# Kernel tuning notes

Hardware: AMD Instinct MI355X
Metric: run time of the kernel (lower is better)

The kernel has to match this reference:

```python
import jax, jax.numpy as jnp
import numpy as np

MEM_SIZE = 2000
FEA_DIM = 256
FMAP = 32
BATCH = 32
SHRINK = 0.0025
EPS = 1e-12


def setup_inputs() -> dict:
    key = jax.random.key(0)
    k1, k2, k3, k4 = jax.random.split(key, 4)
    stdv = 1.0 / np.sqrt(FEA_DIM)
    inp = {
        "input": jax.random.normal(k1, (BATCH, FEA_DIM, FMAP, FMAP), dtype=jnp.float32),
        "label_batch": jax.random.randint(k2, (BATCH,), 0, 2),
        "weight": jax.random.uniform(k3, (MEM_SIZE, FEA_DIM), dtype=jnp.float32, minval=-stdv, maxval=stdv),
        "pos_embedding": jax.random.normal(k4, (1, FEA_DIM, FMAP, FMAP), dtype=jnp.float32),
    }
    return inp


def _forward(x, weight, pos_embedding):
    b, c, h, w = x.shape
    m = weight.shape[0]
    x = x + pos_embedding  # pos=True
    xr = x.transpose(0, 2, 3, 1).reshape(-1, c)  # [b*h*w, c]
    # addressing: linear -> softmax over memory slots
    att = jax.nn.softmax(jnp.einsum('nc,mc->nm', xr, weight), axis=1)  # [N, m]
    # compact loss: MSE to nearest memory item (argmax of att before shrink)
    idx = jnp.argmax(att, axis=1)
    pos_item = weight[idx]  # [N, c]
    compact_loss = jnp.mean((xr - pos_item) ** 2)
    # distance loss: hinge on pairwise squared distances between memory items
    sq = jnp.sum(weight * weight, axis=1)
    d2 = sq[:, None] + sq[None, :] - 2.0 * (weight @ weight.T)  # [m, m]
    dist = 1.0 - d2
    dist = dist * (dist > 0).astype(dist.dtype)
    dist = jnp.triu(dist, k=1)
    distance_loss = dist.sum() * 2.0 / (m * (m - 1))
    # hard shrink relu + L1 normalize (shrink_thres > 0)
    att = jax.nn.relu(att - SHRINK) * att / (jnp.abs(att - SHRINK) + EPS)
    att = att / jnp.maximum(jnp.sum(jnp.abs(att), axis=1, keepdims=True), EPS)
    # memory read
    out = jnp.einsum('nm,mc->nc', att, weight)
    out = out.reshape(b, h, w, c).transpose(0, 3, 1, 2)
    return out, compact_loss, distance_loss


def reference(input, label_batch, weight, pos_embedding):
    return _forward(input, weight, pos_embedding)
```

## Files before the change

kernel.cpp:

```cpp
#include <hip/hip_runtime.h>
#include <hip/hip_bf16.h>

typedef unsigned char u8;
typedef unsigned short u16;
typedef unsigned int u32;
typedef long long s64;
typedef float f32x4 __attribute__((ext_vector_type(4)));
typedef long long s64x2 __attribute__((ext_vector_type(2)));

#define MEM    2000
#define FEA    256
#define SLSTR  2064
#define OSTR   265
#define XRS    264
#define XRBASE 98304
#define RING2  66048
#define POOLSZ 131584
#define OUTN   8388608

typedef const __attribute__((address_space(1))) u32* gp1;
typedef __attribute__((address_space(3))) u32* lp3;

__device__ __forceinline__ void gl_lds16(const void* g, void* l) {
    __builtin_amdgcn_global_load_lds((gp1)g, (lp3)l, 16, 0, 0);
}
__device__ __forceinline__ void pipe_bar() {
    __builtin_amdgcn_sched_barrier(0);
    __builtin_amdgcn_s_barrier();
    __builtin_amdgcn_sched_barrier(0);
}
__device__ __forceinline__ void lds_bar() {
    asm volatile("s_waitcnt lgkmcnt(0)" ::: "memory");
    pipe_bar();
}

__device__ __forceinline__ u32 f2e4m3(float x) {
    float ax = fabsf(x);
    u32 s = (__builtin_bit_cast(u32, x) >> 24) & 0x80u;
    if (ax >= 448.f) return s | 0x7e;
    if (ax < 0.015625f) {
        int q = (int)rintf(ax * 512.f);
        return s | (u32)q;
    }
    int e = (int)(__builtin_bit_cast(u32, ax) >> 23) - 127;
    float scale = __builtin_bit_cast(float, (u32)((127 - e + 3) << 23));
    int q = (int)rintf(ax * scale);
    int E = e + 7;
    if (q == 16) { q = 8; E += 1; if (E > 15) return s | 0x7e; }
    return s | (u32)(E << 3) | (u32)(q & 7);
}
__device__ __forceinline__ u32 f2e4m3_fast(float v) {
    u32 u = __builtin_bit_cast(u32, v);
    u += 0x0007FFFFu + ((u >> 20) & 1u);
    int bb = (int)(u >> 20) - 0x3C0;
    return bb < 0 ? 0u : (u32)bb;
}

__global__ __launch_bounds__(256) void prep_kernel(const float* __restrict__ W,
                                                   u8* __restrict__ WTc,
                                                   u8* __restrict__ Wc,
                                                   float* __restrict__ sqv,
                                                   float* __restrict__ loss) {
    const int blk = blockIdx.x, t = threadIdx.x;
    const int m0 = blk * 8;
    {
        const int sl = t >> 5, cl = t & 31;
        const int slot = m0 + sl;
        const int ch0 = cl * 8;
        const float* wr = W + slot * 256 + ch0;
        f32x4 v0 = *(const f32x4*)wr;
        f32x4 v1 = *(const f32x4*)(wr + 4);
        float ss = v0[0]*v0[0] + v0[1]*v0[1] + v0[2]*v0[2] + v0[3]*v0[3]
                 + v1[0]*v1[0] + v1[1]*v1[1] + v1[2]*v1[2] + v1[3]*v1[3];
        ss += __shfl_xor(ss, 1); ss += __shfl_xor(ss, 2); ss += __shfl_xor(ss, 4);
        ss += __shfl_xor(ss, 8); ss += __shfl_xor(ss, 16);
        if (cl == 0) sqv[slot] = ss;
        const int c = slot >> 6, s = slot & 63;
        const int kk = cl >> 2, agp = cl & 3;
        const int kp = kk >> 1, klo = kk & 1;
        u32 lo = 0, hi = 0;
#pragma unroll
        for (int i = 0; i < 4; ++i) {
            lo |= f2e4m3(v0[i] * 16.f) << (i * 8);
            hi |= f2e4m3(v1[i] * 16.f) << (i * 8);
        }
        u8* dst = Wc + c * 16384 + (size_t)((kp * 4 + agp) * 64 + s) * 16 + klo * 8;
        *(u32*)dst = lo;
        *(u32*)(dst + 4) = hi;
    }
    {
        const int ch = t;
        const int chunk = m0 >> 6, kl0 = m0 & 63;
        u32 lo = 0, hi = 0;
#pragma unroll
        for (int i = 0; i < 8; ++i) {
            u32 bb = f2e4m3(W[(m0 + i) * 256 + ch] * 16.f);
            if (i < 4) lo |= bb << (i * 8); else hi |= bb << ((i - 4) * 8);
        }
        u8* dst = WTc + chunk * 16384 + ch * 64 + (kl0 ^ ((ch & 7) << 3));
        *(u32*)dst = lo;
        *(u32*)(dst + 4) = hi;
    }
    if (blk == 0 && t == 0) {
        loss[0] = 0.0f;
        loss[1] = -2000.0f / (2000.0f * 1999.0f);
    }
}

__global__ __launch_bounds__(512, 1) void main_kernel(
        const float* __restrict__ inp, const float* __restrict__ posb,
        const u8* __restrict__ Wc, const u8* __restrict__ WTc,
        const float* __restrict__ sqv, float* __restrict__ out,
        float* __restrict__ loss) {
    __shared__ __align__(16) u8 pool[POOLSZ];
    __shared__ float sPM[4][32];
    __shared__ int   sPI[4][32];
    __shared__ float sPZ[4][32];
    __shared__ float sPD[4][32];
    __shared__ float sSS[8][32];
    __shared__ float sMax[32];
    __shared__ float sThr[32];
    __shared__ float sInv[32];

    const int t = threadIdx.x;
    const int w = t >> 6, lane = t & 63;
    const int ar = lane & 15, ag = lane >> 4;
    const int blk = blockIdx.x, b = blk >> 5, hw0 = (blk & 31) << 5;
    const int prot = ((blk >> 3) & 15) * 2;
    const int q = w & 3, rt = w >> 2;
    const int row_a = rt * 16 + ar;

#pragma unroll
    for (int cl = 0; cl < 4; ++cl) {
        const int pc = (cl + prot) & 31;
        const u8* src = Wc + pc * 16384 + w * 2048 + lane * 16;
        u8* dst = pool + (cl % 6) * 16384 + w * 2048;
        gl_lds16(src, dst);
        gl_lds16(src + 1024, dst + 1024);
    }

    {
        const int hw = t & 31, cg = t >> 5;
        const float* ip = inp + (size_t)b * 262144 + hw0 + hw;
        const float* pp = posb + hw0 + hw;
        float ss = 0.f;
        u8* xrow = pool + XRBASE + hw * XRS + cg * 16;
#pragma unroll
        for (int j = 0; j < 8; ++j) {
            const int ch = cg * 16 + 2 * j;
            float v0 = ip[ch * 1024] + pp[ch * 1024];
            float v1 = ip[(ch + 1) * 1024] + pp[(ch + 1) * 1024];
            ss += v0 * v0 + v1 * v1;
            u16 pk2 = (u16)(f2e4m3(v0 * 4.f) | (f2e4m3(v1 * 4.f) << 8));
            *(u16*)(xrow + 2 * j) = pk2;
        }
        ss += __shfl_xor(ss, 32);
        if (lane < 32) sSS[w][lane] = ss;
    }
    lds_bar();

    s64 xB[8];
#pragma unroll
    for (int kk = 0; kk < 8; ++kk)
        xB[kk] = *(const s64*)(pool + XRBASE + row_a * XRS + kk * 32 + ag * 8);
    asm volatile("s_waitcnt lgkmcnt(0)" ::: "memory");
    __builtin_amdgcn_sched_barrier(0);

    f32x4 acc[32];
    const int c31 = (31 - prot) & 31;
    {
        const int rowoff = (q * 16 + ar) * 16;
#pragma unroll
        for (int i = 0; i < 16; ++i) {
            if (i <= 14) asm volatile("s_waitcnt vmcnt(4)" ::: "memory");
            else         asm volatile("s_waitcnt vmcnt(0)" ::: "memory");
            pipe_bar();
            if (i <= 13) {
#pragma unroll
                for (int u = 0; u < 2; ++u) {
                    const int cl = 2 * i + 4 + u;
                    const int pc = (cl + prot) & 31;
                    const u8* src = Wc + pc * 16384 + w * 2048 + lane * 16;
                    u8* dst = pool + (cl % 6) * 16384 + w * 2048;
                    gl_lds16(src, dst);
                    gl_lds16(src + 1024, dst + 1024);
                }
            }
#pragma unroll
            for (int u = 0; u < 2; ++u) {
                const int cl = 2 * i + u;
                const u8* base = pool + (cl % 6) * 16384 + rowoff;
                f32x4 a = {0.f, 0.f, 0.f, 0.f};
#pragma unroll
                for (int kp = 0; kp < 4; ++kp) {
                    s64x2 wA = *(const s64x2*)(base + (kp * 4 + ag) * 1024);
                    a = __builtin_amdgcn_mfma_f32_16x16x32_fp8_fp8(wA[0], xB[2 * kp], a, 0, 0, 0);
                    a = __builtin_amdgcn_mfma_f32_16x16x32_fp8_fp8(wA[1], xB[2 * kp + 1], a, 0, 0, 0);
                }
                if (cl == c31 && q != 0) { a[0] = -3e38f; a[1] = -3e38f; a[2] = -3e38f; a[3] = -3e38f; }
                acc[cl] = a;
            }
        }
    }

    {
        float bm = -3e38f; int bi = 0x7fffffff;
#pragma unroll
        for (int c = 0; c < 32; ++c) {
            const int cb = (((c + prot) & 31) << 6) + q * 16 + ag * 4;
#pragma unroll
            for (int e = 0; e < 4; ++e) {
                float f = acc[c][e];
                int id = cb + e;
                if (f > bm || (f == bm && id < bi)) { bm = f; bi = id; }
            }
        }
#pragma unroll
        for (int d = 16; d < 64; d <<= 1) {
            float om = __shfl_xor(bm, d);
            int   oi = __shfl_xor(bi, d);
            if (om > bm || (om == bm && oi < bi)) { bm = om; bi = oi; }
        }
        if (lane < 16) { sPM[q][rt * 16 + lane] = bm; sPI[q][rt * 16 + lane] = bi; }
    }

#pragma unroll
    for (int u = 0; u < 2; ++u) {
        const int pc = (u + prot) & 31;
        const u8* src = WTc + pc * 16384 + w * 2048 + lane * 16;
        u8* dst = pool + RING2 + u * 16384 + w * 2048;
        gl_lds16(src, dst);
        gl_lds16(src + 1024, dst + 1024);
    }
    lds_bar();

    if (t < 32) {
        float mx = sPM[0][t]; int bid = sPI[0][t];
#pragma unroll
        for (int qq = 1; qq < 4; ++qq) {
            float m2 = sPM[qq][t]; int i2 = sPI[qq][t];
            if (m2 > mx || (m2 == mx && i2 < bid)) { mx = m2; bid = i2; }
        }
        sMax[t] = mx;
        float ssq = 0.f;
#pragma unroll
        for (int ww = 0; ww < 8; ++ww) ssq += sSS[ww][t];
        float term = ssq - 2.f * (mx * 0.015625f) + sqv[bid];
#pragma unroll
        for (int d = 1; d < 32; d <<= 1) term += __shfl_xor(term, d);
        if (t == 0) atomicAdd(loss, term * (1.0f / 8388608.0f));
    }
    lds_bar();

    {
        const float mxv = sMax[row_a];
        float z = 0.f;
#pragma unroll
        for (int c = 0; c < 32; ++c)
#pragma unroll
            for (int e = 0; e < 4; ++e) {
                float a_ = __expf((acc[c][e] - mxv) * 0.015625f);
                acc[c][e] = a_;
                z += a_;
            }
        z += __shfl_xor(z, 16); z += __shfl_xor(z, 32);
        if (lane < 16) sPZ[q][rt * 16 + lane] = z;
    }
    lds_bar();
    if (t < 32) sThr[t] = 0.0025f * (sPZ[0][t] + sPZ[1][t] + sPZ[2][t] + sPZ[3][t]);
    lds_bar();

    {
        const float thrv = sThr[row_a];
        const int newoff = (((q * 2 + (ag >> 1)) & 3) << 4) | ((q >> 1) << 3) | ((ag & 1) << 2);
        const int rowbase = row_a * SLSTR + newoff;
        float den = 0.f;
#pragma unroll
        for (int c = 0; c < 32; ++c) {
            const int off = rowbase + (((c + prot) & 31) << 6);
            u32 pk = 0;
#pragma unroll
            for (int e = 0; e < 4; ++e) {
                float a_ = acc[c][e];
                if (a_ > thrv) { den += a_; pk |= f2e4m3_fast(a_ * 64.f) << (e * 8); }
            }
            *(u32*)(pool + off) = pk;
        }
        den += __shfl_xor(den, 16); den += __shfl_xor(den, 32);
        if (lane < 16) sPD[q][rt * 16 + lane] = den;
    }
    lds_bar();
    if (t < 32) {
        float dd = sPD[0][t] + sPD[1][t] + sPD[2][t] + sPD[3][t];
        sInv[t] = dd > 0.f ? 1.0f / (1024.0f * dd) : 0.0f;
    }
    lds_bar();

    const int ch0 = (w * 2) * 16 + ar;
    const int ch1 = ch0 + 16;
    int bo[2][2];
#pragma unroll
    for (int kk = 0; kk < 2; ++kk) {
        bo[0][kk] = (ch0 * 64 + kk * 32 + ag * 8) ^ ((ch0 & 7) << 3);
        bo[1][kk] = (ch1 * 64 + kk * 32 + ag * 8) ^ ((ch1 & 7) << 3);
    }
    const u8* sLr0 = pool + ar * SLSTR + ag * 16;
    const u8* sLr1 = pool + (16 + ar) * SLSTR + ag * 16;
    f32x4 o00 = {0.f,0.f,0.f,0.f}, o01 = {0.f,0.f,0.f,0.f};
    f32x4 o10 = {0.f,0.f,0.f,0.f}, o11 = {0.f,0.f,0.f,0.f};
#pragma unroll
    for (int i = 0; i < 16; ++i) {
        asm volatile("s_waitcnt vmcnt(0)" ::: "memory");
        pipe_bar();
        if (i < 15) {
#pragma unroll
            for (int u = 0; u < 2; ++u) {
                const int cl = 2 * i + 2 + u;
                const int pc = (cl + prot) & 31;
                const u8* src = WTc + pc * 16384 + w * 2048 + lane * 16;
                u8* dst = pool + RING2 + (cl & 3) * 16384 + w * 2048;
                gl_lds16(src, dst);
                gl_lds16(src + 1024, dst + 1024);
            }
        }
#pragma unroll
        for (int u = 0; u < 2; ++u) {
            const int cl = 2 * i + u;
            const u8* base = pool + RING2 + (cl & 3) * 16384;
            const int cc64 = ((cl + prot) & 31) << 6;
            s64x2 A0 = *(const s64x2*)(sLr0 + cc64);
            s64x2 A1 = *(const s64x2*)(sLr1 + cc64);
            s64 B00 = *(const s64*)(base + bo[0][0]);
            s64 B01 = *(const s64*)(base + bo[0][1]);
            s64 B10 = *(const s64*)(base + bo[1][0]);
            s64 B11 = *(const s64*)(base + bo[1][1]);
            o00 = __builtin_amdgcn_mfma_f32_16x16x32_fp8_fp8(A0[0], B00, o00, 0, 0, 0);
            o00 = __builtin_amdgcn_mfma_f32_16x16x32_fp8_fp8(A0[1], B01, o00, 0, 0, 0);
            o01 = __builtin_amdgcn_mfma_f32_16x16x32_fp8_fp8(A1[0], B00, o01, 0, 0, 0);
            o01 = __builtin_amdgcn_mfma_f32_16x16x32_fp8_fp8(A1[1], B01, o01, 0, 0, 0);
            o10 = __builtin_amdgcn_mfma_f32_16x16x32_fp8_fp8(A0[0], B10, o10, 0, 0, 0);
            o10 = __builtin_amdgcn_mfma_f32_16x16x32_fp8_fp8(A0[1], B11, o10, 0, 0, 0);
            o11 = __builtin_amdgcn_mfma_f32_16x16x32_fp8_fp8(A1[0], B10, o11, 0, 0, 0);
            o11 = __builtin_amdgcn_mfma_f32_16x16x32_fp8_fp8(A1[1], B11, o11, 0, 0, 0);
        }
    }
    lds_bar();

    {
        float* sO = (float*)pool;
#pragma unroll
        for (int i = 0; i < 4; ++i) {
            int r0 = ag * 4 + i, r1 = 16 + ag * 4 + i;
            sO[r0 * OSTR + ch0] = o00[i] * sInv[r0];
            sO[r1 * OSTR + ch0] = o01[i] * sInv[r1];
            sO[r0 * OSTR + ch1] = o10[i] * sInv[r0];
            sO[r1 * OSTR + ch1] = o11[i] * sInv[r1];
        }
    }
    lds_bar();
    {
        const float* sO = (const float*)pool;
        const int hw = t & 31, cq = t >> 5;
        float* op = out + (size_t)b * 262144 + hw0 + hw;
#pragma unroll
        for (int i = 0; i < 16; ++i) {
            int ch = cq + (i << 4);
            op[ch * 1024] = sO[hw * OSTR + ch];
        }
    }
}

__global__ __launch_bounds__(256) void dist_kernel(const u8* __restrict__ Wc,
                                                   const float* __restrict__ sqv,
                                                   float* __restrict__ dl) {
    __shared__ float red[4];
    int t = threadIdx.x, w = t >> 6, lane = t & 63;
    int ar = lane & 15, ag = lane >> 4;
    const int i0 = blockIdx.x << 4;
    const int ci = i0 >> 6, si0 = i0 & 63;
    s64x2 af2[4];
#pragma unroll
    for (int kp = 0; kp < 4; ++kp)
        af2[kp] = *(const s64x2*)(Wc + ci * 16384 + (size_t)((kp * 4 + ag) * 64 + si0 + ar) * 16);
    float sqi[4];
#pragma unroll
    for (int e = 0; e < 4; ++e) sqi[e] = sqv[i0 + ag * 4 + e];
    float sum = 0.f;
    for (int jt = w; jt < 125; jt += 4) {
        const int j0 = jt << 4;
        const int cj = j0 >> 6, sj0 = j0 & 63;
        f32x4 acc = {0.f, 0.f, 0.f, 0.f};
#pragma unroll
        for (int kp = 0; kp < 4; ++kp) {
            s64x2 bf = *(const s64x2*)(Wc + cj * 16384 + (size_t)((kp * 4 + ag) * 64 + sj0 + ar) * 16);
            acc = __builtin_amdgcn_mfma_f32_16x16x32_fp8_fp8(af2[kp][0], bf[0], acc, 0, 0, 0);
            acc = __builtin_amdgcn_mfma_f32_16x16x32_fp8_fp8(af2[kp][1], bf[1], acc, 0, 0, 0);
        }
        float sqj = sqv[j0 + ar];
#pragma unroll
        for (int e = 0; e < 4; ++e) {
            float dist = 1.0f - (sqi[e] + sqj - acc[e] * 0.0078125f);
            sum += dist > 0.f ? dist : 0.f;
        }
    }
#pragma unroll
    for (int d = 1; d < 64; d <<= 1) sum += __shfl_xor(sum, d);
    if (lane == 0) red[w] = sum;
    __syncthreads();
    if (t == 0) {
        float s = red[0] + red[1] + red[2] + red[3];
        atomicAdd(dl, s * (1.0f / (2000.0f * 1999.0f)));
    }
}

extern "C" void kernel_launch(void* const* d_in, const int* in_sizes, int n_in,
                              void* d_out, int out_size, void* d_ws, size_t ws_size,
                              hipStream_t stream) {
    (void)in_sizes; (void)n_in; (void)out_size; (void)ws_size;
    const float* inp  = (const float*)d_in[0];
    const float* W    = (const float*)d_in[2];
    const float* posb = (const float*)d_in[3];
    float* out = (float*)d_out;

    u8* WTc = (u8*)d_ws;
    u8* Wc  = (u8*)d_ws + 524288;
    float* sqv = (float*)((u8*)d_ws + 1048576);

    hipLaunchKernelGGL(prep_kernel, dim3(250), dim3(256), 0, stream, W, WTc, Wc, sqv, out + OUTN);
    hipLaunchKernelGGL(main_kernel, dim3(1024), dim3(512), 0, stream, inp, posb, Wc, WTc, sqv, out, out + OUTN);
    hipLaunchKernelGGL(dist_kernel, dim3(125), dim3(256), 0, stream, Wc, sqv, out + OUTN + 1);
}
```

Before: 174.3 us.

## Replace LDS-staged weight pipelines with direct global loads into MFMA operands

Removes the global_load_lds ring buffers that streamed the fp8 weight chunks through shared memory for both GEMMs. Each wave now reads its weight fragments straight from global memory, relying on L2/cache, and the WTc layout changes so the transpose operand is contiguous per lane instead of XOR-swizzled. Shared memory shrinks to about half, which could allow higher occupancy, but this loses explicit prefetch overlap and duplicates weight reads across waves.

```diff
diff --git a/kernel.cpp b/kernel.cpp
--- a/kernel.cpp
+++ b/kernel.cpp
@@ -13,26 +13,8 @@
 #define SLSTR  2064
 #define OSTR   265
 #define XRS    264
-#define XRBASE 98304
-#define RING2  66048
-#define POOLSZ 131584
+#define POOLSZ 66048
 #define OUTN   8388608
-
-typedef const __attribute__((address_space(1))) u32* gp1;
-typedef __attribute__((address_space(3))) u32* lp3;
-
-__device__ __forceinline__ void gl_lds16(const void* g, void* l) {
-    __builtin_amdgcn_global_load_lds((gp1)g, (lp3)l, 16, 0, 0);
-}
-__device__ __forceinline__ void pipe_bar() {
-    __builtin_amdgcn_sched_barrier(0);
-    __builtin_amdgcn_s_barrier();
-    __builtin_amdgcn_sched_barrier(0);
-}
-__device__ __forceinline__ void lds_bar() {
-    asm volatile("s_waitcnt lgkmcnt(0)" ::: "memory");
-    pipe_bar();
-}
 
 __device__ __forceinline__ u32 f2e4m3(float x) {
     float ax = fabsf(x);
@@ -90,14 +72,16 @@
     }
     {
         const int ch = t;
-        const int chunk = m0 >> 6, kl0 = m0 & 63;
+        const int chunk = m0 >> 6;
+        const int kl0 = m0 & 63;
+        const int klo = kl0 >> 5, agp = (kl0 & 31) >> 3;
         u32 lo = 0, hi = 0;
 #pragma unroll
         for (int i = 0; i < 8; ++i) {
             u32 bb = f2e4m3(W[(m0 + i) * 256 + ch] * 16.f);
             if (i < 4) lo |= bb << (i * 8); else hi |= bb << ((i - 4) * 8);
         }
-        u8* dst = WTc + chunk * 16384 + ch * 64 + (kl0 ^ ((ch & 7) << 3));
+        u8* dst = WTc + chunk * 16384 + ch * 64 + agp * 16 + klo * 8;
         *(u32*)dst = lo;
         *(u32*)(dst + 4) = hi;
     }
@@ -130,21 +114,12 @@
     const int q = w & 3, rt = w >> 2;
     const int row_a = rt * 16 + ar;
 
-#pragma unroll
-    for (int cl = 0; cl < 4; ++cl) {
-        const int pc = (cl + prot) & 31;
-        const u8* src = Wc + pc * 16384 + w * 2048 + lane * 16;
-        u8* dst = pool + (cl % 6) * 16384 + w * 2048;
-        gl_lds16(src, dst);
-        gl_lds16(src + 1024, dst + 1024);
-    }
-
     {
         const int hw = t & 31, cg = t >> 5;
         const float* ip = inp + (size_t)b * 262144 + hw0 + hw;
         const float* pp = posb + hw0 + hw;
         float ss = 0.f;
-        u8* xrow = pool + XRBASE + hw * XRS + cg * 16;
+        u8* xrow = pool + hw * XRS + cg * 16;
 #pragma unroll
         for (int j = 0; j < 8; ++j) {
             const int ch = cg * 16 + 2 * j;
@@ -157,49 +132,36 @@
         ss += __shfl_xor(ss, 32);
         if (lane < 32) sSS[w][lane] = ss;
     }
-    lds_bar();
+    __syncthreads();
 
     s64 xB[8];
 #pragma unroll
     for (int kk = 0; kk < 8; ++kk)
-        xB[kk] = *(const s64*)(pool + XRBASE + row_a * XRS + kk * 32 + ag * 8);
-    asm volatile("s_waitcnt lgkmcnt(0)" ::: "memory");
-    __builtin_amdgcn_sched_barrier(0);
+        xB[kk] = *(const s64*)(pool + row_a * XRS + kk * 32 + ag * 8);
 
     f32x4 acc[32];
     const int c31 = (31 - prot) & 31;
     {
-        const int rowoff = (q * 16 + ar) * 16;
-#pragma unroll
-        for (int i = 0; i < 16; ++i) {
-            if (i <= 14) asm volatile("s_waitcnt vmcnt(4)" ::: "memory");
-            else         asm volatile("s_waitcnt vmcnt(0)" ::: "memory");
-            pipe_bar();
-            if (i <= 13) {
-#pragma unroll
-                for (int u = 0; u < 2; ++u) {
-                    const int cl = 2 * i + 4 + u;
-                    const int pc = (cl + prot) & 31;
-                    const u8* src = Wc + pc * 16384 + w * 2048 + lane * 16;
-                    u8* dst = pool + (cl % 6) * 16384 + w * 2048;
-                    gl_lds16(src, dst);
-                    gl_lds16(src + 1024, dst + 1024);
-                }
-            }
-#pragma unroll
-            for (int u = 0; u < 2; ++u) {
-                const int cl = 2 * i + u;
-                const u8* base = pool + (cl % 6) * 16384 + rowoff;
-                f32x4 a = {0.f, 0.f, 0.f, 0.f};
-#pragma unroll
-                for (int kp = 0; kp < 4; ++kp) {
-                    s64x2 wA = *(const s64x2*)(base + (kp * 4 + ag) * 1024);
-                    a = __builtin_amdgcn_mfma_f32_16x16x32_fp8_fp8(wA[0], xB[2 * kp], a, 0, 0, 0);
-                    a = __builtin_amdgcn_mfma_f32_16x16x32_fp8_fp8(wA[1], xB[2 * kp + 1], a, 0, 0, 0);
-                }
-                if (cl == c31 && q != 0) { a[0] = -3e38f; a[1] = -3e38f; a[2] = -3e38f; a[3] = -3e38f; }
-                acc[cl] = a;
-            }
+        const u8* wbase = Wc + ag * 1024 + (q * 16 + ar) * 16;
+#pragma unroll
+        for (int c = 0; c < 32; ++c) {
+            const int pc = (c + prot) & 31;
+            const u8* p = wbase + pc * 16384;
+            s64x2 w0 = *(const s64x2*)(p);
+            s64x2 w1 = *(const s64x2*)(p + 4096);
+            s64x2 w2 = *(const s64x2*)(p + 8192);
+            s64x2 w3 = *(const s64x2*)(p + 12288);
+            f32x4 a = {0.f, 0.f, 0.f, 0.f};
+            a = __builtin_amdgcn_mfma_f32_16x16x32_fp8_fp8(w0[0], xB[0], a, 0, 0, 0);
+            a = __builtin_amdgcn_mfma_f32_16x16x32_fp8_fp8(w0[1], xB[1], a, 0, 0, 0);
+            a = __builtin_amdgcn_mfma_f32_16x16x32_fp8_fp8(w1[0], xB[2], a, 0, 0, 0);
+            a = __builtin_amdgcn_mfma_f32_16x16x32_fp8_fp8(w1[1], xB[3], a, 0, 0, 0);
+            a = __builtin_amdgcn_mfma_f32_16x16x32_fp8_fp8(w2[0], xB[4], a, 0, 0, 0);
+            a = __builtin_amdgcn_mfma_f32_16x16x32_fp8_fp8(w2[1], xB[5], a, 0, 0, 0);
+            a = __builtin_amdgcn_mfma_f32_16x16x32_fp8_fp8(w3[0], xB[6], a, 0, 0, 0);
+            a = __builtin_amdgcn_mfma_f32_16x16x32_fp8_fp8(w3[1], xB[7], a, 0, 0, 0);
+            if (c == c31 && q != 0) { a[0] = -3e38f; a[1] = -3e38f; a[2] = -3e38f; a[3] = -3e38f; }
+            acc[c] = a;
         }
     }
 
@@ -223,16 +185,7 @@
         }
         if (lane < 16) { sPM[q][rt * 16 + lane] = bm; sPI[q][rt * 16 + lane] = bi; }
     }
-
-#pragma unroll
-    for (int u = 0; u < 2; ++u) {
-        const int pc = (u + prot) & 31;
-        const u8* src = WTc + pc * 16384 + w * 2048 + lane * 16;
-        u8* dst = pool + RING2 + u * 16384 + w * 2048;
-        gl_lds16(src, dst);
-        gl_lds16(src + 1024, dst + 1024);
-    }
-    lds_bar();
+    __syncthreads();
 
     if (t < 32) {
         float mx = sPM[0][t]; int bid = sPI[0][t];
@@ -250,7 +203,7 @@
         for (int d = 1; d < 32; d <<= 1) term += __shfl_xor(term, d);
         if (t == 0) atomicAdd(loss, term * (1.0f / 8388608.0f));
     }
-    lds_bar();
+    __syncthreads();
 
     {
         const float mxv = sMax[row_a];
@@ -266,9 +219,9 @@
         z += __shfl_xor(z, 16); z += __shfl_xor(z, 32);
         if (lane < 16) sPZ[q][rt * 16 + lane] = z;
     }
-    lds_bar();
+    __syncthreads();
     if (t < 32) sThr[t] = 0.0025f * (sPZ[0][t] + sPZ[1][t] + sPZ[2][t] + sPZ[3][t]);
-    lds_bar();
+    __syncthreads();
 
     {
         const float thrv = sThr[row_a];
@@ -289,62 +242,39 @@
         den += __shfl_xor(den, 16); den += __shfl_xor(den, 32);
         if (lane < 16) sPD[q][rt * 16 + lane] = den;
     }
-    lds_bar();
+    __syncthreads();
     if (t < 32) {
         float dd = sPD[0][t] + sPD[1][t] + sPD[2][t] + sPD[3][t];
         sInv[t] = dd > 0.f ? 1.0f / (1024.0f * dd) : 0.0f;
     }
-    lds_bar();
+    __syncthreads();
 
     const int ch0 = (w * 2) * 16 + ar;
     const int ch1 = ch0 + 16;
-    int bo[2][2];
-#pragma unroll
-    for (int kk = 0; kk < 2; ++kk) {
-        bo[0][kk] = (ch0 * 64 + kk * 32 + ag * 8) ^ ((ch0 & 7) << 3);
-        bo[1][kk] = (ch1 * 64 + kk * 32 + ag * 8) ^ ((ch1 & 7) << 3);
-    }
     const u8* sLr0 = pool + ar * SLSTR + ag * 16;
     const u8* sLr1 = pool + (16 + ar) * SLSTR + ag * 16;
+    const u8* wt0 = WTc + ch0 * 64 + ag * 16;
+    const u8* wt1 = WTc + ch1 * 64 + ag * 16;
     f32x4 o00 = {0.f,0.f,0.f,0.f}, o01 = {0.f,0.f,0.f,0.f};
     f32x4 o10 = {0.f,0.f,0.f,0.f}, o11 = {0.f,0.f,0.f,0.f};
 #pragma unroll
-    for (int i = 0; i < 16; ++i) {
-        asm volatile("s_waitcnt vmcnt(0)" ::: "memory");
-        pipe_bar();
-        if (i < 15) {
-#pragma unroll
-            for (int u = 0; u < 2; ++u) {
-                const int cl = 2 * i + 2 + u;
-                const int pc = (cl + prot) & 31;
-                const u8* src = WTc + pc * 16384 + w * 2048 + lane * 16;
-                u8* dst = pool + RING2 + (cl & 3) * 16384 + w * 2048;
-                gl_lds16(src, dst);
-                gl_lds16(src + 1024, dst + 1024);
-            }
-        }
-#pragma unroll
-        for (int u = 0; u < 2; ++u) {
-            const int cl = 2 * i + u;
-            const u8* base = pool + RING2 + (cl & 3) * 16384;
-            const int cc64 = ((cl + prot) & 31) << 6;
-            s64x2 A0 = *(const s64x2*)(sLr0 + cc64);
-            s64x2 A1 = *(const s64x2*)(sLr1 + cc64);
-            s64 B00 = *(const s64*)(base + bo[0][0]);
-            s64 B01 = *(const s64*)(base + bo[0][1]);
-            s64 B10 = *(const s64*)(base + bo[1][0]);
-            s64 B11 = *(const s64*)(base + bo[1][1]);
-            o00 = __builtin_amdgcn_mfma_f32_16x16x32_fp8_fp8(A0[0], B00, o00, 0, 0, 0);
-            o00 = __builtin_amdgcn_mfma_f32_16x16x32_fp8_fp8(A0[1], B01, o00, 0, 0, 0);
-            o01 = __builtin_amdgcn_mfma_f32_16x16x32_fp8_fp8(A1[0], B00, o01, 0, 0, 0);
-            o01 = __builtin_amdgcn_mfma_f32_16x16x32_fp8_fp8(A1[1], B01, o01, 0, 0, 0);
-            o10 = __builtin_amdgcn_mfma_f32_16x16x32_fp8_fp8(A0[0], B10, o10, 0, 0, 0);
-            o10 = __builtin_amdgcn_mfma_f32_16x16x32_fp8_fp8(A0[1], B11, o10, 0, 0, 0);
-            o11 = __builtin_amdgcn_mfma_f32_16x16x32_fp8_fp8(A1[0], B10, o11, 0, 0, 0);
-            o11 = __builtin_amdgcn_mfma_f32_16x16x32_fp8_fp8(A1[1], B11, o11, 0, 0, 0);
-        }
-    }
-    lds_bar();
+    for (int c = 0; c < 32; ++c) {
+        const int pc = (c + prot) & 31;
+        const int cc64 = pc << 6;
+        s64x2 B0 = *(const s64x2*)(wt0 + pc * 16384);
+        s64x2 B1 = *(const s64x2*)(wt1 + pc * 16384);
+        s64x2 A0 = *(const s64x2*)(sLr0 + cc64);
+        s64x2 A1 = *(const s64x2*)(sLr1 + cc64);
+        o00 = __builtin_amdgcn_mfma_f32_16x16x32_fp8_fp8(A0[0], B0[0], o00, 0, 0, 0);
+        o00 = __builtin_amdgcn_mfma_f32_16x16x32_fp8_fp8(A0[1], B0[1], o00, 0, 0, 0);
+        o01 = __builtin_amdgcn_mfma_f32_16x16x32_fp8_fp8(A1[0], B0[0], o01, 0, 0, 0);
+        o01 = __builtin_amdgcn_mfma_f32_16x16x32_fp8_fp8(A1[1], B0[1], o01, 0, 0, 0);
+        o10 = __builtin_amdgcn_mfma_f32_16x16x32_fp8_fp8(A0[0], B1[0], o10, 0, 0, 0);
+        o10 = __builtin_amdgcn_mfma_f32_16x16x32_fp8_fp8(A0[1], B1[1], o10, 0, 0, 0);
+        o11 = __builtin_amdgcn_mfma_f32_16x16x32_fp8_fp8(A1[0], B1[0], o11, 0, 0, 0);
+        o11 = __builtin_amdgcn_mfma_f32_16x16x32_fp8_fp8(A1[1], B1[1], o11, 0, 0, 0);
+    }
+    __syncthreads();
 
     {
         float* sO = (float*)pool;
@@ -357,7 +287,7 @@
             sO[r1 * OSTR + ch1] = o11[i] * sInv[r1];
         }
     }
-    lds_bar();
+    __syncthreads();
     {
         const float* sO = (const float*)pool;
         const int hw = t & 31, cq = t >> 5;
```

New measurement: 169.2 us. -2.9%, faster.
